# Optimization experiments

Measured on AMD Instinct MI355X. Metric: run time of the kernel, lower is better.

## Reference

```python
import jax, jax.numpy as jnp
import numpy as np

N, D, E_LOCAL, E_GLOBAL = 50000, 128, 500000, 600000


def gcn_conv(x, W, b, src, dst, w, n):
    """PyG GCNConv with add_self_loops=True, symmetric normalization.

    deg[i] = sum of incoming edge weights at i + 1 (self-loop weight 1)
    norm_e = deg^-1/2[src] * w_e * deg^-1/2[dst]
    out[i] = sum_e norm_e * (xW)[src_e]  +  deg^-1[i] * (xW)[i]  + b
    """
    xw = x @ W  # [n, out]
    deg = jax.ops.segment_sum(w, dst, num_segments=n) + 1.0
    dinv = jnp.where(deg > 0, jax.lax.rsqrt(deg), 0.0)
    norm = dinv[src] * w * dinv[dst]  # [E]
    agg = jax.ops.segment_sum(norm[:, None] * xw[src], dst, num_segments=n)
    self_loop = (dinv * dinv)[:, None] * xw
    return agg + self_loop + b


def setup_inputs() -> dict:
    key = jax.random.key(0)
    ks = jax.random.split(key, 10)
    activity = jax.random.normal(ks[0], (N, D), dtype=jnp.float32)
    learning = jax.random.normal(ks[1], (N, D), dtype=jnp.float32)
    edge_index = jax.random.randint(ks[2], (2, E_LOCAL), 0, N, dtype=jnp.int32)
    edge_weight = jax.random.uniform(ks[3], (E_LOCAL,), dtype=jnp.float32)
    global_edge_index = jax.random.randint(ks[4], (2, E_GLOBAL), 0, N, dtype=jnp.int32)
    global_edge_weight = jax.random.uniform(ks[5], (E_GLOBAL,), dtype=jnp.float32)
    s = 1.0 / np.sqrt(D)
    W_local = jax.random.uniform(ks[6], (D, D), jnp.float32, -s, s)
    b_local = jnp.zeros((D,), jnp.float32)
    W_global = jax.random.uniform(ks[7], (D, D), jnp.float32, -s, s)
    b_global = jnp.zeros((D,), jnp.float32)
    return {
        "activity": activity, "learning": learning,
        "edge_index": edge_index, "edge_weight": edge_weight,
        "global_edge_index": global_edge_index, "global_edge_weight": global_edge_weight,
        "W_local": W_local, "b_local": b_local,
        "W_global": W_global, "b_global": b_global,
    }


def reference(activity, learning, edge_index, edge_weight,
              global_edge_index, global_edge_weight,
              W_local, b_local, W_global, b_global):
    n = activity.shape[0]
    xa = activity + learning
    # Note: GCNConv1 branches in the original are dead code (outputs overwritten);
    # only GCNConv2 (local and global) affect the output.
    xl = gcn_conv(xa, W_local, b_local, edge_index[0], edge_index[1], edge_weight, n)
    xg = gcn_conv(xa, W_global, b_global, global_edge_index[0], global_edge_index[1], global_edge_weight, n)
    wei = jax.nn.sigmoid(xl + xg)
    return 2.0 * activity * wei + 2.0 * learning * (1.0 - wei)
```

## Files before the change

kernel.cpp:

```cpp
#include <hip/hip_runtime.h>

#define DFEAT 128

typedef __attribute__((ext_vector_type(8))) short short8;
typedef __attribute__((ext_vector_type(4))) float float4v;

__device__ __forceinline__ float bf2f(unsigned int h) {
    union { unsigned int u; float f; } v; v.u = h << 16; return v.f;
}
__device__ __forceinline__ unsigned short f2bf(float f) {
    union { float f; unsigned int u; } v; v.f = f;
    unsigned int u = v.u;
    unsigned int lsb = (u >> 16) & 1u;
    u += 0x7fffu + lsb;
    return (unsigned short)(u >> 16);
}
__device__ __forceinline__ float blo(unsigned int u) {
    union { unsigned int x; float f; } v; v.x = u << 16; return v.f;
}
__device__ __forceinline__ float bhi(unsigned int u) {
    union { unsigned int x; float f; } v; v.x = u & 0xffff0000u; return v.f;
}

__global__ __launch_bounds__(256) void zprep_kernel(
    const float* __restrict__ Wl, const float* __restrict__ Wg,
    unsigned short* __restrict__ WT,
    unsigned int* __restrict__ dc, int nz)
{
    if (blockIdx.x < 128) {
        int idx = blockIdx.x * 256 + threadIdx.x;
        int m = idx >> 14, rem = idx & 16383;
        int k = rem >> 7, c = rem & 127;
        const float* W = m ? Wg : Wl;
        WT[m * 16384 + c * 128 + k] = f2bf(W[k * 128 + c]);
        return;
    }
    int i = (blockIdx.x - 128) * 256 + threadIdx.x;
    if (i < nz) dc[i] = 0u;
}

__global__ __launch_bounds__(256) void gemm_hist_kernel(
    const float* __restrict__ A, const float* __restrict__ L,
    const unsigned short* __restrict__ WT,
    unsigned short* __restrict__ xwl, unsigned short* __restrict__ xwg,
    const int* __restrict__ dstL, const float* __restrict__ wL,
    const int* __restrict__ dstG, const float* __restrict__ wG,
    unsigned int* __restrict__ dc, unsigned short* __restrict__ lp16,
    int El, int Eg, int n, int GB)
{
    if (blockIdx.x >= GB) {
        int e = (blockIdx.x - GB) * 256 + threadIdx.x;
        if (e < El) {
            int t = dstL[e];
            unsigned int add = (1u << 24) | (unsigned int)(wL[e] * 0x1p18f + 0.5f);
            unsigned int old = atomicAdd(&dc[t], add);
            lp16[e] = (unsigned short)(old >> 24);
        } else if (e < El + Eg) {
            int e2 = e - El;
            int t = dstG[e2];
            unsigned int add = (1u << 24) | (unsigned int)(wG[e2] * 0x1p18f + 0.5f);
            unsigned int old = atomicAdd(&dc[n + t], add);
            lp16[e] = (unsigned short)(old >> 24);
        }
        return;
    }
    const int tid  = threadIdx.x;
    const int wid  = tid >> 6;
    const int lane = tid & 63;
    const int quad = lane >> 4;
    const int cl   = lane & 15;

    int rowa = blockIdx.x * 64 + wid * 16 + cl;
    if (rowa > n - 1) rowa = n - 1;

    const float* Ar = A + (size_t)rowa * DFEAT;
    const float* Lr = L + (size_t)rowa * DFEAT;

    short8 a[4];
    #pragma unroll
    for (int kk = 0; kk < 4; ++kk) {
        const int kb = kk * 32 + quad * 8;
        float4 a0 = *(const float4*)&Ar[kb];
        float4 a1 = *(const float4*)&Ar[kb + 4];
        float4 l0 = *(const float4*)&Lr[kb];
        float4 l1 = *(const float4*)&Lr[kb + 4];
        union { short8 v; unsigned short u[8]; } s;
        s.u[0] = f2bf(a0.x + l0.x); s.u[1] = f2bf(a0.y + l0.y);
        s.u[2] = f2bf(a0.z + l0.z); s.u[3] = f2bf(a0.w + l0.w);
        s.u[4] = f2bf(a1.x + l1.x); s.u[5] = f2bf(a1.y + l1.y);
        s.u[6] = f2bf(a1.z + l1.z); s.u[7] = f2bf(a1.w + l1.w);
        a[kk] = s.v;
    }

    const int rbase = blockIdx.x * 64 + wid * 16 + quad * 4;
    const char* wtb = (const char*)WT + quad * 16;

    #pragma unroll
    for (int m = 0; m < 2; ++m) {
        unsigned short* out = m ? xwg : xwl;
        #pragma unroll
        for (int t = 0; t < 8; ++t) {
            const int col = t * 16 + cl;
            const char* bp = wtb + m * 32768 + col * 256;
            float4v acc = {0.f, 0.f, 0.f, 0.f};
            #pragma unroll
            for (int kk = 0; kk < 4; ++kk) {
                short8 b = *(const short8*)(bp + kk * 64);
                acc = __builtin_amdgcn_mfma_f32_16x16x32_bf16(a[kk], b, acc, 0, 0, 0);
            }
            #pragma unroll
            for (int r = 0; r < 4; ++r) {
                int ro = rbase + r;
                if (ro < n) out[(size_t)ro * DFEAT + col] = f2bf(acc[r]);
            }
        }
    }
}

__global__ __launch_bounds__(256) void scan1_kernel(const unsigned int* __restrict__ dc,
                                                    unsigned int* __restrict__ ptrpk,
                                                    float* __restrict__ dinv,
                                                    int* __restrict__ gcount,
                                                    int n2)
{
    __shared__ int tmp[256];
    __shared__ int sbase;
    int i = blockIdx.x * 256 + threadIdx.x;
    int v = 0;
    if (i < n2) {
        unsigned int d = dc[i];
        v = (int)(d >> 24);
        dinv[i] = rsqrtf((float)(d & 0xFFFFFFu) * 0x1p-18f + 1.0f);
    }
    tmp[threadIdx.x] = v;
    __syncthreads();
    for (int off = 1; off < 256; off <<= 1) {
        int t = (threadIdx.x >= off) ? tmp[threadIdx.x - off] : 0;
        __syncthreads();
        tmp[threadIdx.x] += t;
        __syncthreads();
    }
    if (threadIdx.x == 255) sbase = atomicAdd(gcount, tmp[255]);
    __syncthreads();
    if (i < n2)
        ptrpk[i] = (unsigned int)(sbase + tmp[threadIdx.x] - v) | ((unsigned int)v << 24);
}

__global__ __launch_bounds__(256) void edata_write_kernel(
    const int* __restrict__ srcL, const int* __restrict__ dstL, const float* __restrict__ wL,
    const int* __restrict__ srcG, const int* __restrict__ dstG, const float* __restrict__ wG,
    const float* __restrict__ dinv, const unsigned int* __restrict__ ptrpk,
    const unsigned short* __restrict__ lp16, int2* __restrict__ edata,
    int El, int Eg, int n)
{
    int e = blockIdx.x * 256 + threadIdx.x;
    if (e < El) {
        int s = srcL[e], t = dstL[e];
        float norm = dinv[s] * wL[e] * dinv[t];
        int pos = (int)(ptrpk[t] & 0xFFFFFFu) + lp16[e];
        edata[pos] = make_int2(__float_as_int(norm), s);
    } else if (e < El + Eg) {
        int e2 = e - El;
        int s = srcG[e2], t = dstG[e2];
        float norm = dinv[n + s] * wG[e2] * dinv[n + t];
        int pos = (int)(ptrpk[n + t] & 0xFFFFFFu) + lp16[e];
        edata[pos] = make_int2(__float_as_int(norm), s);
    }
}

__global__ __launch_bounds__(256) void gather_kernel(
    const unsigned short* __restrict__ xwl, const unsigned short* __restrict__ xwg,
    const unsigned int* __restrict__ ptrpk, const int2* __restrict__ edata,
    const float* __restrict__ dinv,
    const float* __restrict__ A, const float* __restrict__ Lr,
    const float* __restrict__ bl, const float* __restrict__ bg,
    float* __restrict__ out, int n)
{
    const int lane = threadIdx.x & 63;
    const int grp  = lane >> 4;
    const int fl   = lane & 15;
    const int node = blockIdx.x * 4 + (threadIdx.x >> 6);
    if (node >= n) return;

    const unsigned int pl = ptrpk[node];
    const unsigned int pg = ptrpk[n + node];
    const int i0l = (int)(pl & 0xFFFFFFu);
    const int i1l = i0l + (int)(pl >> 24);
    const int i0g = (int)(pg & 0xFFFFFFu);
    const int i1g = i0g + (int)(pg >> 24);
    float dl = dinv[node];     dl *= dl;
    float dg = dinv[n + node]; dg *= dg;

    const int fo = fl * 8;
    const size_t nbase = (size_t)node * DFEAT + fo;
    const uint4 svl = *(const uint4*)&xwl[nbase];
    const uint4 svg = *(const uint4*)&xwg[nbase];

    float acc[8] = {0.f, 0.f, 0.f, 0.f, 0.f, 0.f, 0.f, 0.f};

    for (int b0 = i0l; b0 < i1l; b0 += 64) {
        int idx = b0 + lane;
        int2 ed = edata[idx < i1l ? idx : (i1l - 1)];
        float nmv = __int_as_float(ed.x);
        int   sv  = ed.y;
        int cnt = i1l - b0; if (cnt > 64) cnt = 64;
        int iters = (cnt + 3) >> 2;
        #pragma unroll 4
        for (int jj = 0; jj < iters; ++jj) {
            int sl = 4 * jj + grp;
            float nm = __shfl(nmv, sl);
            int   s  = __shfl(sv,  sl);
            if (sl >= cnt) nm = 0.f;
            uint4 pk = *(const uint4*)&xwl[(size_t)s * DFEAT + fo];
            acc[0] += nm * blo(pk.x); acc[1] += nm * bhi(pk.x);
            acc[2] += nm * blo(pk.y); acc[3] += nm * bhi(pk.y);
            acc[4] += nm * blo(pk.z); acc[5] += nm * bhi(pk.z);
            acc[6] += nm * blo(pk.w); acc[7] += nm * bhi(pk.w);
        }
    }
    for (int b0 = i0g; b0 < i1g; b0 += 64) {
        int idx = b0 + lane;
        int2 ed = edata[idx < i1g ? idx : (i1g - 1)];
        float nmv = __int_as_float(ed.x);
        int   sv  = ed.y;
        int cnt = i1g - b0; if (cnt > 64) cnt = 64;
        int iters = (cnt + 3) >> 2;
        #pragma unroll 4
        for (int jj = 0; jj < iters; ++jj) {
            int sl = 4 * jj + grp;
            float nm = __shfl(nmv, sl);
            int   s  = __shfl(sv,  sl);
            if (sl >= cnt) nm = 0.f;
            uint4 pk = *(const uint4*)&xwg[(size_t)s * DFEAT + fo];
            acc[0] += nm * blo(pk.x); acc[1] += nm * bhi(pk.x);
            acc[2] += nm * blo(pk.y); acc[3] += nm * bhi(pk.y);
            acc[4] += nm * blo(pk.z); acc[5] += nm * bhi(pk.z);
            acc[6] += nm * blo(pk.w); acc[7] += nm * bhi(pk.w);
        }
    }

    #pragma unroll
    for (int j = 0; j < 8; ++j) {
        acc[j] += __shfl_xor(acc[j], 16);
        acc[j] += __shfl_xor(acc[j], 32);
    }

    acc[0] += dl * blo(svl.x) + dg * blo(svg.x);
    acc[1] += dl * bhi(svl.x) + dg * bhi(svg.x);
    acc[2] += dl * blo(svl.y) + dg * blo(svg.y);
    acc[3] += dl * bhi(svl.y) + dg * bhi(svg.y);
    acc[4] += dl * blo(svl.z) + dg * blo(svg.z);
    acc[5] += dl * bhi(svl.z) + dg * bhi(svg.z);
    acc[6] += dl * blo(svl.w) + dg * blo(svg.w);
    acc[7] += dl * bhi(svl.w) + dg * bhi(svg.w);

    float s0a = (grp & 1) ? acc[2] : acc[0];
    float s1a = (grp & 1) ? acc[3] : acc[1];
    float s0b = (grp & 1) ? acc[6] : acc[4];
    float s1b = (grp & 1) ? acc[7] : acc[5];
    float v0 = (grp & 2) ? s0b : s0a;
    float v1 = (grp & 2) ? s1b : s1a;

    const int f0 = fo + grp * 2;
    const size_t obase = (size_t)node * DFEAT + f0;
    float2 b1 = *(const float2*)&bl[f0];
    float2 b2 = *(const float2*)&bg[f0];
    float2 a2 = *(const float2*)&A[obase];
    float2 l2 = *(const float2*)&Lr[obase];
    v0 += b1.x + b2.x;
    v1 += b1.y + b2.y;
    float w0 = 1.0f / (1.0f + __expf(-v0));
    float w1 = 1.0f / (1.0f + __expf(-v1));
    float o0 = 2.0f * (a2.x * w0 + l2.x * (1.0f - w0));
    float o1 = 2.0f * (a2.y * w1 + l2.y * (1.0f - w1));
    *(float2*)&out[obase] = make_float2(o0, o1);
}

extern "C" void kernel_launch(void* const* d_in, const int* in_sizes, int n_in,
                              void* d_out, int out_size, void* d_ws, size_t ws_size,
                              hipStream_t stream)
{
    const float* activity = (const float*)d_in[0];
    const float* learning = (const float*)d_in[1];
    const int*   ei  = (const int*)d_in[2];
    const float* ew  = (const float*)d_in[3];
    const int*   gei = (const int*)d_in[4];
    const float* gew = (const float*)d_in[5];
    const float* Wl  = (const float*)d_in[6];
    const float* bl  = (const float*)d_in[7];
    const float* Wg  = (const float*)d_in[8];
    const float* bg  = (const float*)d_in[9];

    const int n  = in_sizes[0] / DFEAT;
    const int El = in_sizes[3];
    const int Eg = in_sizes[5];
    const int n2 = 2 * n;
    const int E  = El + Eg;

    char* ws = (char*)d_ws;
    const size_t xwBytes = (size_t)n * DFEAT * 2;

    unsigned short* xwl  = (unsigned short*)ws;
    unsigned short* xwg  = (unsigned short*)(ws + xwBytes);
    float*          dinv = (float*)(ws + 2 * xwBytes);
    unsigned int*   ptrpk= (unsigned int*)(ws + 2 * xwBytes + (size_t)n2 * 4);
    unsigned short* WT   = (unsigned short*)(ws + 2 * xwBytes + (size_t)n2 * 8);
    int2*           edata= (int2*)(ws + 2 * xwBytes + (size_t)n2 * 8 + 65536);
    unsigned short* lp16 = (unsigned short*)(ws + 2 * xwBytes + (size_t)n2 * 8 + 65536
                                             + (size_t)E * 8);
    unsigned int*   dc   = (unsigned int*)(ws + 2 * xwBytes + (size_t)n2 * 8 + 65536
                                             + (size_t)E * 8 + (size_t)((E + 1) & ~1) * 2);
    int* gcount = (int*)(dc + n2);

    const int nz = n2 + 1;
    const int zb = (nz + 255) / 256;
    const int GB = (n + 63) / 64;
    const int HB = (E + 255) / 256;
    const int scanBlocks = (n2 + 255) / 256;

    zprep_kernel<<<dim3(128 + zb), dim3(256), 0, stream>>>(Wl, Wg, WT, dc, nz);

    gemm_hist_kernel<<<dim3(GB + HB), dim3(256), 0, stream>>>(
        activity, learning, WT, xwl, xwg,
        ei + El, ew, gei + Eg, gew, dc, lp16, El, Eg, n, GB);

    scan1_kernel<<<dim3(scanBlocks), dim3(256), 0, stream>>>(dc, ptrpk, dinv, gcount, n2);

    edata_write_kernel<<<dim3(HB), dim3(256), 0, stream>>>(
        ei, ei + El, ew, gei, gei + Eg, gew, dinv, ptrpk, lp16, edata, El, Eg, n);

    gather_kernel<<<dim3((n + 3) / 4), dim3(256), 0, stream>>>(
        xwl, xwg, ptrpk, edata, dinv, activity, learning, bl, bg, (float*)d_out, n);
}
```

Before: 256.5 us.

## Replace global-atomic CSR build with two-level bin sort and packed edge payload

Replaces the per-edge global atomic histogram and scatter with a two-level counting sort. Edges are first binned by destination/256 using shared-memory counts per 4096-edge chunk, then scanned and scattered into bins, then sorted within each bin in shared memory, which also computes degrees and dinv. Each edge entry is packed into 32 bits (16-bit source index and 16-bit quantized weight), and the normalization is recomputed inside the gather. This removes contended global atomics and halves edge storage, but adds more kernel launches, relies on n fitting in 16 bits and on MAXBINS, and quantizes weights to 16 bits.

```diff
diff --git a/kernel.cpp b/kernel.cpp
--- a/kernel.cpp
+++ b/kernel.cpp
@@ -1,6 +1,8 @@
 #include <hip/hip_runtime.h>
 
 #define DFEAT 128
+#define EPB 4096
+#define MAXBINS 512
 
 typedef __attribute__((ext_vector_type(8))) short short8;
 typedef __attribute__((ext_vector_type(4))) float float4v;
@@ -25,7 +27,7 @@
 __global__ __launch_bounds__(256) void zprep_kernel(
     const float* __restrict__ Wl, const float* __restrict__ Wg,
     unsigned short* __restrict__ WT,
-    unsigned int* __restrict__ dc, int nz)
+    unsigned int* __restrict__ counts, int nz)
 {
     if (blockIdx.x < 128) {
         int idx = blockIdx.x * 256 + threadIdx.x;
@@ -36,32 +38,36 @@
         return;
     }
     int i = (blockIdx.x - 128) * 256 + threadIdx.x;
-    if (i < nz) dc[i] = 0u;
-}
-
-__global__ __launch_bounds__(256) void gemm_hist_kernel(
+    if (i < nz) counts[i] = 0u;
+}
+
+__global__ __launch_bounds__(256) void gemm_bin1_kernel(
     const float* __restrict__ A, const float* __restrict__ L,
     const unsigned short* __restrict__ WT,
     unsigned short* __restrict__ xwl, unsigned short* __restrict__ xwg,
-    const int* __restrict__ dstL, const float* __restrict__ wL,
-    const int* __restrict__ dstG, const float* __restrict__ wG,
-    unsigned int* __restrict__ dc, unsigned short* __restrict__ lp16,
-    int El, int Eg, int n, int GB)
-{
+    const int* __restrict__ dstL, const int* __restrict__ dstG,
+    unsigned int* __restrict__ counts,
+    int El, int Eg, int n, int GB, int NPB)
+{
+    __shared__ unsigned int lcnt[MAXBINS];
     if (blockIdx.x >= GB) {
-        int e = (blockIdx.x - GB) * 256 + threadIdx.x;
-        if (e < El) {
-            int t = dstL[e];
-            unsigned int add = (1u << 24) | (unsigned int)(wL[e] * 0x1p18f + 0.5f);
-            unsigned int old = atomicAdd(&dc[t], add);
-            lp16[e] = (unsigned short)(old >> 24);
-        } else if (e < El + Eg) {
-            int e2 = e - El;
-            int t = dstG[e2];
-            unsigned int add = (1u << 24) | (unsigned int)(wG[e2] * 0x1p18f + 0.5f);
-            unsigned int old = atomicAdd(&dc[n + t], add);
-            lp16[e] = (unsigned short)(old >> 24);
+        const int NBINS = (2 * n + 255) >> 8;
+        for (int b = threadIdx.x; b < NBINS; b += 256) lcnt[b] = 0u;
+        __syncthreads();
+        const int k = blockIdx.x - GB;
+        const int e0 = k * EPB;
+        const int E = El + Eg;
+        #pragma unroll
+        for (int r = 0; r < EPB / 256; ++r) {
+            int e = e0 + r * 256 + threadIdx.x;
+            if (e < E) {
+                int t = (e < El) ? dstL[e] : n + dstG[e - El];
+                atomicAdd(&lcnt[t >> 8], 1u);
+            }
         }
+        __syncthreads();
+        for (int b = threadIdx.x; b < NBINS; b += 256)
+            counts[(size_t)b * NPB + k] = lcnt[b];
         return;
     }
     const int tid  = threadIdx.x;
@@ -117,60 +123,124 @@
     }
 }
 
-__global__ __launch_bounds__(256) void scan1_kernel(const unsigned int* __restrict__ dc,
-                                                    unsigned int* __restrict__ ptrpk,
-                                                    float* __restrict__ dinv,
-                                                    int* __restrict__ gcount,
-                                                    int n2)
-{
-    __shared__ int tmp[256];
-    __shared__ int sbase;
-    int i = blockIdx.x * 256 + threadIdx.x;
-    int v = 0;
-    if (i < n2) {
-        unsigned int d = dc[i];
-        v = (int)(d >> 24);
-        dinv[i] = rsqrtf((float)(d & 0xFFFFFFu) * 0x1p-18f + 1.0f);
-    }
-    tmp[threadIdx.x] = v;
-    __syncthreads();
-    for (int off = 1; off < 256; off <<= 1) {
-        int t = (threadIdx.x >= off) ? tmp[threadIdx.x - off] : 0;
-        __syncthreads();
-        tmp[threadIdx.x] += t;
-        __syncthreads();
-    }
-    if (threadIdx.x == 255) sbase = atomicAdd(gcount, tmp[255]);
-    __syncthreads();
-    if (i < n2)
-        ptrpk[i] = (unsigned int)(sbase + tmp[threadIdx.x] - v) | ((unsigned int)v << 24);
-}
-
-__global__ __launch_bounds__(256) void edata_write_kernel(
+__global__ __launch_bounds__(512) void scanA_kernel(unsigned int* __restrict__ counts,
+                                                    unsigned int* __restrict__ bintot,
+                                                    int NPB)
+{
+    __shared__ unsigned int tmp[512];
+    const int b = blockIdx.x;
+    const int i = threadIdx.x;
+    unsigned int v = (i < NPB) ? counts[(size_t)b * NPB + i] : 0u;
+    tmp[i] = v;
+    __syncthreads();
+    for (int off = 1; off < 512; off <<= 1) {
+        unsigned int t = (i >= off) ? tmp[i - off] : 0u;
+        __syncthreads();
+        tmp[i] += t;
+        __syncthreads();
+    }
+    if (i < NPB) counts[(size_t)b * NPB + i] = tmp[i] - v;
+    if (i == 511) bintot[b] = tmp[511];
+}
+
+__global__ __launch_bounds__(512) void scanB_kernel(const unsigned int* __restrict__ bintot,
+                                                    unsigned int* __restrict__ binbase,
+                                                    int NBINS)
+{
+    __shared__ unsigned int tmp[512];
+    const int i = threadIdx.x;
+    unsigned int v = (i < NBINS) ? bintot[i] : 0u;
+    tmp[i] = v;
+    __syncthreads();
+    for (int off = 1; off < 512; off <<= 1) {
+        unsigned int t = (i >= off) ? tmp[i - off] : 0u;
+        __syncthreads();
+        tmp[i] += t;
+        __syncthreads();
+    }
+    if (i < NBINS) binbase[i] = tmp[i] - v;
+    if (i == 511) binbase[NBINS] = tmp[511];
+}
+
+__global__ __launch_bounds__(256) void scatter_kernel(
     const int* __restrict__ srcL, const int* __restrict__ dstL, const float* __restrict__ wL,
     const int* __restrict__ srcG, const int* __restrict__ dstG, const float* __restrict__ wG,
-    const float* __restrict__ dinv, const unsigned int* __restrict__ ptrpk,
-    const unsigned short* __restrict__ lp16, int2* __restrict__ edata,
-    int El, int Eg, int n)
-{
-    int e = blockIdx.x * 256 + threadIdx.x;
-    if (e < El) {
-        int s = srcL[e], t = dstL[e];
-        float norm = dinv[s] * wL[e] * dinv[t];
-        int pos = (int)(ptrpk[t] & 0xFFFFFFu) + lp16[e];
-        edata[pos] = make_int2(__float_as_int(norm), s);
-    } else if (e < El + Eg) {
-        int e2 = e - El;
-        int s = srcG[e2], t = dstG[e2];
-        float norm = dinv[n + s] * wG[e2] * dinv[n + t];
-        int pos = (int)(ptrpk[n + t] & 0xFFFFFFu) + lp16[e];
-        edata[pos] = make_int2(__float_as_int(norm), s);
+    const unsigned int* __restrict__ counts, const unsigned int* __restrict__ binbase,
+    unsigned int* __restrict__ payload, unsigned char* __restrict__ tloc,
+    int El, int Eg, int n, int NPB)
+{
+    __shared__ unsigned int lbase[MAXBINS];
+    __shared__ unsigned int lcnt[MAXBINS];
+    const int NBINS = (2 * n + 255) >> 8;
+    const int k = blockIdx.x;
+    for (int b = threadIdx.x; b < NBINS; b += 256) {
+        lbase[b] = binbase[b] + counts[(size_t)b * NPB + k];
+        lcnt[b]  = 0u;
+    }
+    __syncthreads();
+    const int e0 = k * EPB;
+    const int E = El + Eg;
+    #pragma unroll
+    for (int r = 0; r < EPB / 256; ++r) {
+        int e = e0 + r * 256 + threadIdx.x;
+        if (e < E) {
+            int s, t; float w;
+            if (e < El) { s = srcL[e]; t = dstL[e]; w = wL[e]; }
+            else { int e2 = e - El; s = srcG[e2]; t = n + dstG[e2]; w = wG[e2]; }
+            const int bin = t >> 8;
+            unsigned int rank = atomicAdd(&lcnt[bin], 1u);
+            unsigned int pos = lbase[bin] + rank;
+            unsigned int wq = (unsigned int)(w * 65535.0f + 0.5f);
+            if (wq > 65535u) wq = 65535u;
+            payload[pos] = (wq << 16) | (unsigned int)s;
+            tloc[pos] = (unsigned char)(t & 255);
+        }
+    }
+}
+
+__global__ __launch_bounds__(256) void binsort_kernel(
+    const unsigned int* __restrict__ binbase,
+    const unsigned int* __restrict__ payload, const unsigned char* __restrict__ tloc,
+    unsigned int* __restrict__ edata, unsigned int* __restrict__ ptrpk,
+    float* __restrict__ dinv, int n2)
+{
+    __shared__ unsigned int cnt[256], wsum[256], off[256], cnt2[256], tmp[256];
+    const int b = blockIdx.x;
+    const unsigned int s0 = binbase[b], s1 = binbase[b + 1];
+    cnt[threadIdx.x] = 0u; wsum[threadIdx.x] = 0u; cnt2[threadIdx.x] = 0u;
+    __syncthreads();
+    for (unsigned int i = s0 + threadIdx.x; i < s1; i += 256) {
+        unsigned int tl = tloc[i];
+        atomicAdd(&cnt[tl], 1u);
+        atomicAdd(&wsum[tl], payload[i] >> 16);
+    }
+    __syncthreads();
+    unsigned int v = cnt[threadIdx.x];
+    tmp[threadIdx.x] = v;
+    __syncthreads();
+    for (int o = 1; o < 256; o <<= 1) {
+        unsigned int t = (threadIdx.x >= o) ? tmp[threadIdx.x - o] : 0u;
+        __syncthreads();
+        tmp[threadIdx.x] += t;
+        __syncthreads();
+    }
+    off[threadIdx.x] = tmp[threadIdx.x] - v;
+    const int t = b * 256 + threadIdx.x;
+    if (t < n2) {
+        dinv[t]  = rsqrtf((float)wsum[threadIdx.x] * (1.0f / 65535.0f) + 1.0f);
+        ptrpk[t] = (s0 + off[threadIdx.x]) | (v << 24);
+    }
+    __syncthreads();
+    for (unsigned int i = s0 + threadIdx.x; i < s1; i += 256) {
+        unsigned int tl = tloc[i];
+        unsigned int r = atomicAdd(&cnt2[tl], 1u);
+        edata[s0 + off[tl] + r] = payload[i];
     }
 }
 
 __global__ __launch_bounds__(256) void gather_kernel(
     const unsigned short* __restrict__ xwl, const unsigned short* __restrict__ xwg,
-    const unsigned int* __restrict__ ptrpk, const int2* __restrict__ edata,
+    const unsigned int* __restrict__ ptrpk, const unsigned int* __restrict__ edata,
     const float* __restrict__ dinv,
     const float* __restrict__ A, const float* __restrict__ Lr,
     const float* __restrict__ bl, const float* __restrict__ bg,
@@ -188,8 +258,12 @@
     const int i1l = i0l + (int)(pl >> 24);
     const int i0g = (int)(pg & 0xFFFFFFu);
     const int i1g = i0g + (int)(pg >> 24);
-    float dl = dinv[node];     dl *= dl;
-    float dg = dinv[n + node]; dg *= dg;
+    const float dvl = dinv[node];
+    const float dvg = dinv[n + node];
+    const float dl = dvl * dvl;
+    const float dg = dvg * dvg;
+    const float dtl = dvl * (1.0f / 65535.0f);
+    const float dtg = dvg * (1.0f / 65535.0f);
 
     const int fo = fl * 8;
     const size_t nbase = (size_t)node * DFEAT + fo;
@@ -200,9 +274,9 @@
 
     for (int b0 = i0l; b0 < i1l; b0 += 64) {
         int idx = b0 + lane;
-        int2 ed = edata[idx < i1l ? idx : (i1l - 1)];
-        float nmv = __int_as_float(ed.x);
-        int   sv  = ed.y;
+        unsigned int ed = edata[idx < i1l ? idx : (i1l - 1)];
+        int   sv  = (int)(ed & 0xFFFFu);
+        float nmv = dinv[sv] * (float)(ed >> 16) * dtl;
         int cnt = i1l - b0; if (cnt > 64) cnt = 64;
         int iters = (cnt + 3) >> 2;
         #pragma unroll 4
@@ -220,9 +294,9 @@
     }
     for (int b0 = i0g; b0 < i1g; b0 += 64) {
         int idx = b0 + lane;
-        int2 ed = edata[idx < i1g ? idx : (i1g - 1)];
-        float nmv = __int_as_float(ed.x);
-        int   sv  = ed.y;
+        unsigned int ed = edata[idx < i1g ? idx : (i1g - 1)];
+        int   sv  = (int)(ed & 0xFFFFu);
+        float nmv = dinv[n + sv] * (float)(ed >> 16) * dtg;
         int cnt = i1g - b0; if (cnt > 64) cnt = 64;
         int iters = (cnt + 3) >> 2;
         #pragma unroll 4
@@ -297,37 +371,43 @@
     const int n2 = 2 * n;
     const int E  = El + Eg;
 
+    const int NPB   = (E + EPB - 1) / EPB;
+    const int NBINS = (n2 + 255) / 256;
+
     char* ws = (char*)d_ws;
-    const size_t xwBytes = (size_t)n * DFEAT * 2;
-
-    unsigned short* xwl  = (unsigned short*)ws;
-    unsigned short* xwg  = (unsigned short*)(ws + xwBytes);
-    float*          dinv = (float*)(ws + 2 * xwBytes);
-    unsigned int*   ptrpk= (unsigned int*)(ws + 2 * xwBytes + (size_t)n2 * 4);
-    unsigned short* WT   = (unsigned short*)(ws + 2 * xwBytes + (size_t)n2 * 8);
-    int2*           edata= (int2*)(ws + 2 * xwBytes + (size_t)n2 * 8 + 65536);
-    unsigned short* lp16 = (unsigned short*)(ws + 2 * xwBytes + (size_t)n2 * 8 + 65536
-                                             + (size_t)E * 8);
-    unsigned int*   dc   = (unsigned int*)(ws + 2 * xwBytes + (size_t)n2 * 8 + 65536
-                                             + (size_t)E * 8 + (size_t)((E + 1) & ~1) * 2);
-    int* gcount = (int*)(dc + n2);
-
-    const int nz = n2 + 1;
+    const size_t xwB = (size_t)n * DFEAT * 2;
+    size_t off = 0;
+    unsigned short* xwl = (unsigned short*)(ws + off); off += xwB;
+    unsigned short* xwg = (unsigned short*)(ws + off); off += xwB;
+    float* dinv         = (float*)(ws + off);          off += (size_t)n2 * 4;
+    unsigned int* ptrpk = (unsigned int*)(ws + off);   off += (size_t)n2 * 4;
+    unsigned short* WT  = (unsigned short*)(ws + off); off += 65536;
+    unsigned int* payload = (unsigned int*)(ws + off); off += (size_t)E * 4;
+    unsigned char* tloc = (unsigned char*)(ws + off);  off += (size_t)((E + 3) & ~3);
+    unsigned int* edata = (unsigned int*)(ws + off);   off += (size_t)E * 4;
+    unsigned int* counts= (unsigned int*)(ws + off);   off += (size_t)NBINS * NPB * 4;
+    unsigned int* bintot= (unsigned int*)(ws + off);   off += (size_t)NBINS * 4;
+    unsigned int* binbase=(unsigned int*)(ws + off);   off += (size_t)(NBINS + 1) * 4;
+
+    const int nz = NBINS * NPB;
     const int zb = (nz + 255) / 256;
     const int GB = (n + 63) / 64;
-    const int HB = (E + 255) / 256;
-    const int scanBlocks = (n2 + 255) / 256;
-
-    zprep_kernel<<<dim3(128 + zb), dim3(256), 0, stream>>>(Wl, Wg, WT, dc, nz);
-
-    gemm_hist_kernel<<<dim3(GB + HB), dim3(256), 0, stream>>>(
+
+    zprep_kernel<<<dim3(128 + zb), dim3(256), 0, stream>>>(Wl, Wg, WT, counts, nz);
+
+    gemm_bin1_kernel<<<dim3(GB + NPB), dim3(256), 0, stream>>>(
         activity, learning, WT, xwl, xwg,
-        ei + El, ew, gei + Eg, gew, dc, lp16, El, Eg, n, GB);
-
-    scan1_kernel<<<dim3(scanBlocks), dim3(256), 0, stream>>>(dc, ptrpk, dinv, gcount, n2);
-
-    edata_write_kernel<<<dim3(HB), dim3(256), 0, stream>>>(
-        ei, ei + El, ew, gei, gei + Eg, gew, dinv, ptrpk, lp16, edata, El, Eg, n);
+        ei + El, gei + Eg, counts, El, Eg, n, GB, NPB);
+
+    scanA_kernel<<<dim3(NBINS), dim3(512), 0, stream>>>(counts, bintot, NPB);
+    scanB_kernel<<<dim3(1), dim3(512), 0, stream>>>(bintot, binbase, NBINS);
+
+    scatter_kernel<<<dim3(NPB), dim3(256), 0, stream>>>(
+        ei, ei + El, ew, gei, gei + Eg, gew,
+        counts, binbase, payload, tloc, El, Eg, n, NPB);
+
+    binsort_kernel<<<dim3(NBINS), dim3(256), 0, stream>>>(
+        binbase, payload, tloc, edata, ptrpk, dinv, n2);
 
     gather_kernel<<<dim3((n + 3) / 4), dim3(256), 0, stream>>>(
         xwl, xwg, ptrpk, edata, dinv, activity, learning, bl, bg, (float*)d_out, n);
```

New measurement: 255.3 us. Within noise of the previous version (-0.5%).
